# Kernel optimization log

Measured on AMD Instinct MI355X. Metric: run time of the kernel, lower is better.

Reference implementation:

```python
import jax, jax.numpy as jnp
import numpy as np

MD = 4  # maximum displacement


def setup_inputs() -> dict:
    key = jax.random.key(0)
    k0, k1 = jax.random.split(key)
    B, C, H, W = 8, 128, 96, 192
    input0 = jax.random.normal(k0, (B, C, H, W), dtype=jnp.float32)
    input1 = jax.random.normal(k1, (B, C, H, W), dtype=jnp.float32)
    return {"input0": input0, "input1": input1}


def reference(input0, input1):
    # Sliding-window cross-correlation (PWC-Net cost volume).
    # out[b, d, h, w] = (1/C) * sum_c input0[b,c,h,w] * input1_shifted_d[b,c,h,w]
    B, C, H, W = input0.shape
    big1 = jnp.pad(input1, ((0, 0), (0, 0), (MD, MD), (MD, MD)))
    # Fixed small set of (2*MD+1)^2 = 81 displacements; loop is over this
    # structural set, not over data dims.
    outs = [
        jnp.einsum('bchw,bchw->bhw', input0,
                   big1[:, :, MD + r:MD + r + H, MD + c:MD + c + W])
        for r in range(-MD, MD + 1)
        for c in range(-MD, MD + 1)
    ]
    out = jnp.stack(outs, axis=1)  # [B, 81, H, W]
    return out / C
```

## Files before the change

### kernel.cpp

```cpp
#include <hip/hip_runtime.h>

namespace {
constexpr int MD = 4;
constexpr int BB = 8, CC = 128, HH = 96, WW = 192;
constexpr int TH = 4, TW = 64;
constexpr int NROWS = TH + 2 * MD;
constexpr int ROWF  = 80;
constexpr int LSTR  = 84;
constexpr int NF4   = NROWS * (ROWF / 4);
}

__global__ __launch_bounds__(192, 2)
void corr81(const float* __restrict__ in0,
            const float* __restrict__ in1,
            float* __restrict__ out)
{
    const int tid  = threadIdx.x;
    const int wv   = tid >> 6;
    const int lane = tid & 63;
    const int g    = lane >> 4;
    const int q    = lane & 15;

    const int w0 = blockIdx.x * TW;
    const int h0 = blockIdx.y * TH;
    const int b  = blockIdx.z;

    __shared__ float lds[NROWS][LSTR];

    const size_t plane = (size_t)HH * WW;
    const size_t img   = (size_t)CC * plane;

    const float* in1b = in1 + (size_t)b * img;

    const int f0 = tid;
    const int r0 = f0 / 20, c0 = (f0 % 20) * 4;
    const int f1 = tid + 192;
    const int r1 = f1 / 20, c1 = (f1 % 20) * 4;
    const bool has1 = (f1 < NF4);

    const int grow0 = h0 - MD + r0, gcol0 = w0 - 8 + c0;
    const int grow1 = h0 - MD + r1, gcol1 = w0 - 8 + c1;
    const bool ok0 = (grow0 >= 0 && grow0 < HH && gcol0 >= 0 && gcol0 < WW);
    const bool ok1 = has1 && (grow1 >= 0 && grow1 < HH && gcol1 >= 0 && gcol1 < WW);

    const float* p0 = in1b + (size_t)grow0 * WW + gcol0;
    const float* p1 = in1b + (size_t)grow1 * WW + gcol1;
    const float* pa = in0 + (size_t)b * img + (size_t)(h0 + g) * WW + (w0 + q * 4);

    float acc[3][9][4];
    #pragma unroll
    for (int rr = 0; rr < 3; ++rr)
        #pragma unroll
        for (int cc = 0; cc < 9; ++cc)
            #pragma unroll
            for (int j = 0; j < 4; ++j) acc[rr][cc][j] = 0.f;

    float4 s0 = ok0 ? *(const float4*)p0 : make_float4(0.f, 0.f, 0.f, 0.f);
    float4 s1 = ok1 ? *(const float4*)p1 : make_float4(0.f, 0.f, 0.f, 0.f);

    for (int c = 0; c < CC; ++c) {
        __syncthreads();
        *(float4*)&lds[r0][c0] = s0;
        if (has1) *(float4*)&lds[r1][c1] = s1;
        const float4 a = *(const float4*)pa;
        pa += plane;
        __syncthreads();
        if (c + 1 < CC) {
            p0 += plane; p1 += plane;
            s0 = ok0 ? *(const float4*)p0 : make_float4(0.f, 0.f, 0.f, 0.f);
            s1 = ok1 ? *(const float4*)p1 : make_float4(0.f, 0.f, 0.f, 0.f);
        }
        const float av[4] = {a.x, a.y, a.z, a.w};
        #pragma unroll
        for (int rr = 0; rr < 3; ++rr) {
            const int row = g + wv * 3 + rr;
            const float4 wA = *(const float4*)&lds[row][q * 4 + 4];
            const float4 wB = *(const float4*)&lds[row][q * 4 + 8];
            const float4 wC = *(const float4*)&lds[row][q * 4 + 12];
            const float win[12] = {wA.x, wA.y, wA.z, wA.w,
                                   wB.x, wB.y, wB.z, wB.w,
                                   wC.x, wC.y, wC.z, wC.w};
            #pragma unroll
            for (int cc = 0; cc < 9; ++cc)
                #pragma unroll
                for (int j = 0; j < 4; ++j)
                    acc[rr][cc][j] = fmaf(av[j], win[cc + j], acc[rr][cc][j]);
        }
    }

    const float scale = 1.0f / CC;
    float* ob = out + ((size_t)b * 81) * plane + (size_t)(h0 + g) * WW + (w0 + q * 4);
    #pragma unroll
    for (int rr = 0; rr < 3; ++rr) {
        const int dbase = (wv * 3 + rr) * 9;
        #pragma unroll
        for (int cc = 0; cc < 9; ++cc) {
            float4 o = make_float4(acc[rr][cc][0] * scale, acc[rr][cc][1] * scale,
                                   acc[rr][cc][2] * scale, acc[rr][cc][3] * scale);
            *(float4*)(ob + (size_t)(dbase + cc) * plane) = o;
        }
    }
}

extern "C" void kernel_launch(void* const* d_in, const int* in_sizes, int n_in,
                              void* d_out, int out_size, void* d_ws, size_t ws_size,
                              hipStream_t stream)
{
    const float* in0 = (const float*)d_in[0];
    const float* in1 = (const float*)d_in[1];
    float* out = (float*)d_out;
    dim3 grid(WW / TW, HH / TH, BB);
    corr81<<<grid, dim3(192), 0, stream>>>(in0, in1, out);
}
```

Baseline: 107.7 us.

## Stage in1 tiles in chunks of 8 channels per barrier pair

```diff
diff --git a/kernel.cpp b/kernel.cpp
--- a/kernel.cpp
+++ b/kernel.cpp
@@ -4,13 +4,18 @@
 constexpr int MD = 4;
 constexpr int BB = 8, CC = 128, HH = 96, WW = 192;
 constexpr int TH = 4, TW = 64;
+constexpr int KC = 8;
+constexpr int NCHUNK = CC / KC;
 constexpr int NROWS = TH + 2 * MD;
 constexpr int ROWF  = 80;
 constexpr int LSTR  = 84;
-constexpr int NF4   = NROWS * (ROWF / 4);
+constexpr int F4_PER_ROW = ROWF / 4;
+constexpr int F4_PER_CH  = NROWS * F4_PER_ROW;
+constexpr int NTHR = 192;
+constexpr int PER_THR = KC * F4_PER_CH / NTHR;
 }
 
-__global__ __launch_bounds__(192, 2)
+__global__ __launch_bounds__(NTHR, 2)
 void corr81(const float* __restrict__ in0,
             const float* __restrict__ in1,
             float* __restrict__ out)
@@ -25,26 +30,29 @@
     const int h0 = blockIdx.y * TH;
     const int b  = blockIdx.z;
 
-    __shared__ float lds[NROWS][LSTR];
+    __shared__ float lds[KC][NROWS][LSTR];
 
     const size_t plane = (size_t)HH * WW;
     const size_t img   = (size_t)CC * plane;
+    const float* in1b  = in1 + (size_t)b * img;
 
-    const float* in1b = in1 + (size_t)b * img;
+    int  soff[PER_THR];
+    int  loff[PER_THR];
+    bool sok[PER_THR];
+    #pragma unroll
+    for (int i = 0; i < PER_THR; ++i) {
+        const int idx = tid + i * NTHR;
+        const int ch  = idx / F4_PER_CH;
+        const int rem = idx % F4_PER_CH;
+        const int row = rem / F4_PER_ROW;
+        const int col = (rem % F4_PER_ROW) * 4;
+        const int grow = h0 - MD + row;
+        const int gcol = w0 - 8 + col;
+        sok[i]  = (grow >= 0 && grow < HH && gcol >= 0 && gcol < WW);
+        soff[i] = ch * (int)plane + grow * WW + gcol;
+        loff[i] = (int)(((ch * NROWS + row) * LSTR + col) * sizeof(float));
+    }
 
-    const int f0 = tid;
-    const int r0 = f0 / 20, c0 = (f0 % 20) * 4;
-    const int f1 = tid + 192;
-    const int r1 = f1 / 20, c1 = (f1 % 20) * 4;
-    const bool has1 = (f1 < NF4);
-
-    const int grow0 = h0 - MD + r0, gcol0 = w0 - 8 + c0;
-    const int grow1 = h0 - MD + r1, gcol1 = w0 - 8 + c1;
-    const bool ok0 = (grow0 >= 0 && grow0 < HH && gcol0 >= 0 && gcol0 < WW);
-    const bool ok1 = has1 && (grow1 >= 0 && grow1 < HH && gcol1 >= 0 && gcol1 < WW);
-
-    const float* p0 = in1b + (size_t)grow0 * WW + gcol0;
-    const float* p1 = in1b + (size_t)grow1 * WW + gcol1;
     const float* pa = in0 + (size_t)b * img + (size_t)(h0 + g) * WW + (w0 + q * 4);
 
     float acc[3][9][4];
@@ -55,36 +63,48 @@
             #pragma unroll
             for (int j = 0; j < 4; ++j) acc[rr][cc][j] = 0.f;
 
-    float4 s0 = ok0 ? *(const float4*)p0 : make_float4(0.f, 0.f, 0.f, 0.f);
-    float4 s1 = ok1 ? *(const float4*)p1 : make_float4(0.f, 0.f, 0.f, 0.f);
+    float4 stg[PER_THR];
+    #pragma unroll
+    for (int i = 0; i < PER_THR; ++i)
+        stg[i] = sok[i] ? *(const float4*)(in1b + soff[i])
+                        : make_float4(0.f, 0.f, 0.f, 0.f);
 
-    for (int c = 0; c < CC; ++c) {
+    for (int k = 0; k < NCHUNK; ++k) {
         __syncthreads();
-        *(float4*)&lds[r0][c0] = s0;
-        if (has1) *(float4*)&lds[r1][c1] = s1;
-        const float4 a = *(const float4*)pa;
-        pa += plane;
+        #pragma unroll
+        for (int i = 0; i < PER_THR; ++i)
+            *(float4*)((char*)lds + loff[i]) = stg[i];
         __syncthreads();
-        if (c + 1 < CC) {
-            p0 += plane; p1 += plane;
-            s0 = ok0 ? *(const float4*)p0 : make_float4(0.f, 0.f, 0.f, 0.f);
-            s1 = ok1 ? *(const float4*)p1 : make_float4(0.f, 0.f, 0.f, 0.f);
+
+        if (k + 1 < NCHUNK) {
+            const float* nb = in1b + (size_t)(k + 1) * KC * plane;
+            #pragma unroll
+            for (int i = 0; i < PER_THR; ++i)
+                stg[i] = sok[i] ? *(const float4*)(nb + soff[i])
+                                : make_float4(0.f, 0.f, 0.f, 0.f);
         }
-        const float av[4] = {a.x, a.y, a.z, a.w};
+
+        const float* pak = pa + (size_t)k * KC * plane;
         #pragma unroll
-        for (int rr = 0; rr < 3; ++rr) {
-            const int row = g + wv * 3 + rr;
-            const float4 wA = *(const float4*)&lds[row][q * 4 + 4];
-            const float4 wB = *(const float4*)&lds[row][q * 4 + 8];
-            const float4 wC = *(const float4*)&lds[row][q * 4 + 12];
-            const float win[12] = {wA.x, wA.y, wA.z, wA.w,
-                                   wB.x, wB.y, wB.z, wB.w,
-                                   wC.x, wC.y, wC.z, wC.w};
+        for (int ch = 0; ch < KC; ++ch) {
+            const float4 a = *(const float4*)(pak + (size_t)ch * plane);
+            const float av[4] = {a.x, a.y, a.z, a.w};
             #pragma unroll
-            for (int cc = 0; cc < 9; ++cc)
+            for (int rr = 0; rr < 3; ++rr) {
+                const int row = g + wv * 3 + rr;
+                const float* lrow = &lds[ch][row][q * 4];
+                const float4 wA = *(const float4*)(lrow + 4);
+                const float4 wB = *(const float4*)(lrow + 8);
+                const float4 wC = *(const float4*)(lrow + 12);
+                const float win[12] = {wA.x, wA.y, wA.z, wA.w,
+                                       wB.x, wB.y, wB.z, wB.w,
+                                       wC.x, wC.y, wC.z, wC.w};
                 #pragma unroll
-                for (int j = 0; j < 4; ++j)
-                    acc[rr][cc][j] = fmaf(av[j], win[cc + j], acc[rr][cc][j]);
+                for (int cc = 0; cc < 9; ++cc)
+                    #pragma unroll
+                    for (int j = 0; j < 4; ++j)
+                        acc[rr][cc][j] = fmaf(av[j], win[cc + j], acc[rr][cc][j]);
+            }
         }
     }
 
@@ -110,5 +130,5 @@
     const float* in1 = (const float*)d_in[1];
     float* out = (float*)d_out;
     dim3 grid(WW / TW, HH / TH, BB);
-    corr81<<<grid, dim3(192), 0, stream>>>(in0, in1, out);
+    corr81<<<grid, dim3(NTHR), 0, stream>>>(in0, in1, out);
 }
```

Result: slower. 285.6 us (+165.2%).
